# Optimization experiments

Hardware: AMD Instinct MI355X
Metric: run time of the kernel (lower is better)

## Reference

```python
import jax, jax.numpy as jnp
import numpy as np

K_NEIGHBORS = 32  # n_neighbors, eval mode -> displacement = 0


def setup_inputs() -> dict:
    key = jax.random.key(0)
    ks = jax.random.split(key, 9)
    B, N, F = 1024, 200000, 64
    C, H = 16, 128
    return {
        "x": jax.random.normal(ks[0], (B, F), jnp.float32),
        "X_data": jax.random.normal(ks[1], (N, F), jnp.float32),
        "y": jax.random.uniform(ks[2], (N,), jnp.float32),
        "W_gate": jax.random.normal(ks[3], (F + 1, C), jnp.float32) / np.sqrt(F + 1),
        "b_gate": jax.random.normal(ks[4], (C,), jnp.float32) * 0.01,
        "W1": jax.random.normal(ks[5], (C + F, H), jnp.float32) / np.sqrt(C + F),
        "b1": jax.random.normal(ks[6], (H,), jnp.float32) * 0.01,
        "W_last": jax.random.normal(ks[7], (H, 1), jnp.float32) / np.sqrt(H),
        "b_last": jax.random.normal(ks[8], (1,), jnp.float32) * 0.01,
    }


def reference(x, X_data, y, W_gate, b_gate, W1, b1, W_last, b_last):
    # Euclidean (p=2) cdist via the expanded form: ||a-b||^2 = ||a||^2 + ||b||^2 - 2 a.b
    d2 = (jnp.sum(x * x, axis=1, keepdims=True)
          + jnp.sum(X_data * X_data, axis=1)[None, :]
          - 2.0 * (x @ X_data.T))                      # [B, N]
    dist = jnp.sqrt(jnp.maximum(d2, 0.0))
    # torch.argsort(distances,1)[:, :k] == indices of k smallest distances
    _, idx = jax.lax.top_k(-dist, K_NEIGHBORS)          # [B, K]
    neighbors = X_data[idx]                             # [B, K, F] gather
    neighbors_y = y[idx][..., None]                     # [B, K, 1]
    nf = jnp.concatenate([neighbors, neighbors_y], axis=2)  # [B, K, F+1]
    gated = jnp.tanh(nf @ W_gate + b_gate)              # [B, K, C]
    agg = jnp.sum(gated, axis=1)                        # [B, C]
    o = jnp.concatenate([x, agg], axis=1)               # [B, F+C]
    o = jnp.tanh(o @ W1 + b1)                           # activation_function = tanh
    o = jax.nn.sigmoid(o @ W_last + b_last)             # [B, 1]
    return o
```

## Files before the change

### kernel.cpp

```cpp
#include <hip/hip_runtime.h>
#include <cstdint>

#define FDIM 64
#define KNN 32
#define NBUCKET 256
#define MAXCAP 2048
#define SEG 10
#define OCAP 512
#define BANDQ 96

typedef unsigned int u32;
typedef unsigned long long u64;
typedef __attribute__((ext_vector_type(8))) short bf16x8;
typedef __attribute__((ext_vector_type(4))) float f32x4;

__device__ __forceinline__ void gload_lds16(const void* g, void* l) {
    __builtin_amdgcn_global_load_lds(
        (const __attribute__((address_space(1))) unsigned int*)g,
        (__attribute__((address_space(3))) unsigned int*)l,
        16, 0, 0);
}

__device__ __forceinline__ float load_query(const float* __restrict__ x, int q, float4* xv) {
    const float4* xp = (const float4*)(x + (size_t)q * FDIM);
    float n0 = 0.f, n1 = 0.f, n2 = 0.f, n3 = 0.f;
#pragma unroll
    for (int k = 0; k < 16; ++k) {
        float4 v = xp[k];
        xv[k] = v;
        n0 = fmaf(v.x, v.x, n0); n1 = fmaf(v.y, v.y, n1);
        n2 = fmaf(v.z, v.z, n2); n3 = fmaf(v.w, v.w, n3);
    }
    return (n0 + n1) + (n2 + n3);
}

__device__ __forceinline__ float dot_row(const float4* __restrict__ xv, const float* __restrict__ row) {
    const float4* rv = (const float4*)row;
    float d0 = 0.f, d1 = 0.f, d2 = 0.f, d3 = 0.f;
#pragma unroll
    for (int k = 0; k < 16; ++k) {
        float4 r = rv[k];
        float4 a = xv[k];
        d0 = fmaf(a.x, r.x, d0); d1 = fmaf(a.y, r.y, d1);
        d2 = fmaf(a.z, r.z, d2); d3 = fmaf(a.w, r.w, d3);
    }
    return (d0 + d1) + (d2 + d3);
}

__global__ __launch_bounds__(256) void k_xnorm(const float* __restrict__ X, float* __restrict__ Xn, int N) {
    int i = blockIdx.x * 256 + threadIdx.x;
    if (i >= N) return;
    const float4* r = (const float4*)(X + (size_t)i * FDIM);
    float d0 = 0.f, d1 = 0.f, d2 = 0.f, d3 = 0.f;
#pragma unroll
    for (int k = 0; k < 16; ++k) {
        float4 v = r[k];
        d0 = fmaf(v.x, v.x, d0); d1 = fmaf(v.y, v.y, d1);
        d2 = fmaf(v.z, v.z, d2); d3 = fmaf(v.w, v.w, d3);
    }
    Xn[i] = (d0 + d1) + (d2 + d3);
}

__global__ __launch_bounds__(256) void k_cvtT(const float* __restrict__ src, uint4* __restrict__ dst, int n_u4) {
    int i = blockIdx.x * 256 + threadIdx.x;
    if (i >= n_u4) return;
    int lane = i & 63;
    int kk = (i >> 6) & 1;
    int g = i >> 7;
    int row = g * 16 + (lane & 15);
    int col = kk * 32 + (lane >> 4) * 8;
    const float4* s = (const float4*)(src + (size_t)row * FDIM + col);
    float4 a = s[0], b = s[1];
    ushort o[8];
    const float* f = &a.x;
#pragma unroll
    for (int k = 0; k < 4; ++k) {
        u32 u = __float_as_uint(f[k]);
        o[k] = (ushort)((u + 0x7fffu + ((u >> 16) & 1u)) >> 16);
    }
    const float* gg = &b.x;
#pragma unroll
    for (int k = 0; k < 4; ++k) {
        u32 u = __float_as_uint(gg[k]);
        o[4 + k] = (ushort)((u + 0x7fffu + ((u >> 16) & 1u)) >> 16);
    }
    dst[i] = *(uint4*)o;
}

__global__ __launch_bounds__(256) void k_hist(const float* __restrict__ x, const float* __restrict__ X,
                                              const float* __restrict__ Xn, u32* __restrict__ hist,
                                              int N, int nsamp, int sj) {
    __shared__ unsigned char h8[NBUCKET * 256];
    int t = threadIdx.x;
    u32* h32 = (u32*)h8;
#pragma unroll
    for (int k = 0; k < 64; ++k) h32[k * 256 + t] = 0;
    __syncthreads();
    int q = blockIdx.x * 256 + t;
    float4 xv[16];
    float xn = load_query(x, q, xv);
    for (int j = 0; j < sj; ++j) {
        int s = blockIdx.y * sj + j;
        int p = s * 16;
        if (s < nsamp && p < N) {
            float dp = dot_row(xv, X + (size_t)p * FDIM);
            float d2 = fmaxf(xn + Xn[p] - 2.f * dp, 0.f);
            int b = min(NBUCKET - 1, (int)d2);
            int idx = b * 256 + t;
            unsigned char v = h8[idx];
            h8[idx] = (v == 255u) ? v : (unsigned char)(v + 1);
        }
    }
    __syncthreads();
#pragma unroll
    for (int w = 0; w < 128; ++w) {
        u32 v0 = h8[(2 * w) * 256 + t];
        u32 v1 = h8[(2 * w + 1) * 256 + t];
        if (v0 | v1) atomicAdd(&hist[(size_t)q * 128 + w], v0 | (v1 << 16));
    }
}

__global__ __launch_bounds__(256) void k_thresh(const u32* __restrict__ hist, float* __restrict__ Tq, int B) {
    int q = blockIdx.x * 256 + threadIdx.x;
    if (q >= B) return;
    const u32* h = hist + (size_t)q * 128;
    int cum = 0;
    float T = (float)NBUCKET;
    for (int w = 0; w < 128; ++w) {
        u32 v = h[w];
        cum += (int)(v & 0xffffu);
        if (cum >= KNN) { T = (float)(2 * w + 1); break; }
        cum += (int)(v >> 16);
        if (cum >= KNN) { T = (float)(2 * w + 2); break; }
    }
    Tq[q] = T + 2.0f;
}

__global__ __launch_bounds__(256, 3) void k_sample_d2(
        const uint4* __restrict__ xT, const uint4* __restrict__ XT,
        const float* __restrict__ qn, const float* __restrict__ Xn,
        unsigned char* __restrict__ d2s, int S) {
    int t = threadIdx.x;
    int w = t >> 6, lane = t & 63;
    int G = lane >> 4, r = lane & 15;
    int qg = blockIdx.x;
    int wq = qg * 128 + w * 32;
    int pb = blockIdx.y * 128;

    bf16x8 afr[2][2];
#pragma unroll
    for (int kk = 0; kk < 2; ++kk)
#pragma unroll
        for (int mi = 0; mi < 2; ++mi) {
            uint4 v = xT[(size_t)(((wq >> 4) + mi) * 2 + kk) * 64 + lane];
            afr[kk][mi] = *(bf16x8*)&v;
        }
    float qr[8];
#pragma unroll
    for (int e = 0; e < 8; ++e)
        qr[e] = qn[wq + (e >> 2) * 16 + G * 4 + (e & 3)];

#pragma unroll
    for (int half = 0; half < 2; ++half) {
        int nb = half * 4;
        bf16x8 bfr[4][2];
#pragma unroll
        for (int j = 0; j < 4; ++j) {
            int gp = (pb >> 4) + nb + j;
#pragma unroll
            for (int kk = 0; kk < 2; ++kk) {
                uint4 v = XT[(size_t)(gp * 2 + kk) * 64 + lane];
                bfr[j][kk] = *(bf16x8*)&v;
            }
        }
        float xnv[4];
#pragma unroll
        for (int j = 0; j < 4; ++j) xnv[j] = Xn[pb + (nb + j) * 16 + r];

        f32x4 acc[2][4];
#pragma unroll
        for (int mi = 0; mi < 2; ++mi)
#pragma unroll
            for (int j = 0; j < 4; ++j) acc[mi][j] = (f32x4){0.f, 0.f, 0.f, 0.f};
#pragma unroll
        for (int kk = 0; kk < 2; ++kk)
#pragma unroll
            for (int j = 0; j < 4; ++j) {
                acc[0][j] = __builtin_amdgcn_mfma_f32_16x16x32_bf16(afr[kk][0], bfr[j][kk], acc[0][j], 0, 0, 0);
                acc[1][j] = __builtin_amdgcn_mfma_f32_16x16x32_bf16(afr[kk][1], bfr[j][kk], acc[1][j], 0, 0, 0);
            }
#pragma unroll
        for (int j = 0; j < 4; ++j) {
            int p = pb + (nb + j) * 16 + r;
            float xnp = xnv[j];
#pragma unroll
            for (int e = 0; e < 8; ++e) {
                float d2a = qr[e] + fmaf(-2.f, acc[e >> 2][j][e & 3], xnp);
                int b = (int)d2a;
                b = b < 0 ? 0 : (b > 255 ? 255 : b);
                int q = wq + (e >> 2) * 16 + G * 4 + (e & 3);
                d2s[(size_t)q * S + p] = (unsigned char)b;
            }
        }
    }
}

__global__ __launch_bounds__(256) void k_thresh2(const unsigned char* __restrict__ d2s,
                                                 float* __restrict__ Tq, int S) {
    __shared__ u32 h[NBUCKET];
    int t = threadIdx.x;
    int q = blockIdx.x;
    h[t] = 0;
    __syncthreads();
    const u32* row = (const u32*)(d2s + (size_t)q * S);
    int n4 = S >> 2;
    for (int i = t; i < n4; i += 256) {
        u32 v = row[i];
        atomicAdd(&h[v & 255u], 1u);
        atomicAdd(&h[(v >> 8) & 255u], 1u);
        atomicAdd(&h[(v >> 16) & 255u], 1u);
        atomicAdd(&h[v >> 24], 1u);
    }
    __syncthreads();
    if (t == 0) {
        int cum = 0;
        float T = 256.0f;
        for (int b = 0; b < NBUCKET; ++b) {
            cum += (int)h[b];
            if (cum >= KNN) { T = (float)(b + 1); break; }
        }
        Tq[q] = T + 2.0f;
    }
}

__global__ __launch_bounds__(256, 4) void k_mfma_filter(
        const uint4* __restrict__ xT, const uint4* __restrict__ XT,
        const float* __restrict__ qn, const float* __restrict__ Xn,
        const float* __restrict__ Tf,
        u32* __restrict__ cnt_seg, u32* __restrict__ list_seg,
        u32* __restrict__ ocnt, u32* __restrict__ olist,
        int N, int nStripsPad, int strip) {
    __shared__ uint4 sbuf[2][1024];
    __shared__ u32 ldsCnt[128];

    int t = threadIdx.x;
    int w = t >> 6, lane = t & 63;
    int G = lane >> 4, r = lane & 15;

    int bid = blockIdx.x;
    int qg = (bid >> 3) & 7;
    int sIdx = (bid & 7) | ((bid >> 6) << 3);
    int qbase = qg * 128;
    int wq = qbase + w * 32;

    if (t < 128) ldsCnt[t] = 0;
    __syncthreads();

    bf16x8 afr[2][2];
#pragma unroll
    for (int kk = 0; kk < 2; ++kk)
#pragma unroll
        for (int mi = 0; mi < 2; ++mi) {
            uint4 v = xT[(size_t)(((wq >> 4) + mi) * 2 + kk) * 64 + lane];
            afr[kk][mi] = *(bf16x8*)&v;
        }
    float nT[8], qnr[8];
#pragma unroll
    for (int e = 0; e < 8; ++e) {
        int rl = wq + (e >> 2) * 16 + G * 4 + (e & 3);
        float qv = qn[rl];
        qnr[e] = qv;
        nT[e] = -0.5f * (Tf[rl] - qv);
    }

    u32* segBase = list_seg + ((size_t)qbase * nStripsPad + (size_t)sIdx) * SEG;

    int pb0 = sIdx * strip * 128;
    int ntl = (pb0 < N) ? strip : 0;

    if (ntl > 0) {
        {
            const char* src = (const char*)XT + (size_t)(pb0 >> 4) * 2048 + w * 1024 + lane * 16;
            char* dst = (char*)&sbuf[0][0] + w * 1024;
            gload_lds16(src, dst);
            gload_lds16(src + 4096, dst + 4096);
            gload_lds16(src + 8192, dst + 8192);
            gload_lds16(src + 12288, dst + 12288);
        }
        __syncthreads();

        for (int s = 0; s < ntl; ++s) {
            int pb = pb0 + s * 128;
            if (s + 1 < ntl) {
                const char* src = (const char*)XT + (size_t)((pb + 128) >> 4) * 2048 + w * 1024 + lane * 16;
                char* dst = (char*)&sbuf[(s + 1) & 1][0] + w * 1024;
                gload_lds16(src, dst);
                gload_lds16(src + 4096, dst + 4096);
                gload_lds16(src + 8192, dst + 8192);
                gload_lds16(src + 12288, dst + 12288);
            }
            const uint4* cur = &sbuf[s & 1][0];

#pragma unroll
            for (int half = 0; half < 2; ++half) {
                int nb = half * 4;
                bf16x8 bfr[4][2];
#pragma unroll
                for (int j = 0; j < 4; ++j) {
#pragma unroll
                    for (int kk = 0; kk < 2; ++kk) {
                        uint4 v = cur[((nb + j) * 2 + kk) * 64 + lane];
                        bfr[j][kk] = *(bf16x8*)&v;
                    }
                }
                float xnv[4], ai[4];
#pragma unroll
                for (int j = 0; j < 4; ++j) {
                    xnv[j] = Xn[pb + (nb + j) * 16 + r];
                    ai[j] = -0.5f * xnv[j];
                }

                f32x4 acc[2][4];
#pragma unroll
                for (int mi = 0; mi < 2; ++mi)
#pragma unroll
                    for (int j = 0; j < 4; ++j) acc[mi][j] = (f32x4){ai[j], ai[j], ai[j], ai[j]};
#pragma unroll
                for (int kk = 0; kk < 2; ++kk)
#pragma unroll
                    for (int j = 0; j < 4; ++j) {
                        acc[0][j] = __builtin_amdgcn_mfma_f32_16x16x32_bf16(afr[kk][0], bfr[j][kk], acc[0][j], 0, 0, 0);
                        acc[1][j] = __builtin_amdgcn_mfma_f32_16x16x32_bf16(afr[kk][1], bfr[j][kk], acc[1][j], 0, 0, 0);
                    }
#pragma unroll
                for (int j = 0; j < 4; ++j) {
                    int p = pb + (nb + j) * 16 + r;
                    bool ce[8];
#pragma unroll
                    for (int e = 0; e < 8; ++e)
                        ce[e] = acc[e >> 2][j][e & 3] > nT[e];
                    if ((ce[0] | ce[1] | ce[2] | ce[3] | ce[4] | ce[5] | ce[6] | ce[7]) && p < N) {
#pragma unroll
                        for (int e = 0; e < 8; ++e) {
                            if (ce[e]) {
                                float d2a = fmaf(-2.f, acc[e >> 2][j][e & 3], qnr[e]);
                                d2a = d2a < 0.f ? 0.f : d2a;
                                u32 dq = (u32)(d2a * 32.f);
                                if (dq > 16383u) dq = 16383u;
                                u32 key = (dq << 18) | (u32)p;
                                int ql = w * 32 + (e >> 2) * 16 + G * 4 + (e & 3);
                                u32 slot = atomicAdd(&ldsCnt[ql], 1u);
                                if (slot < SEG) {
                                    segBase[(size_t)ql * nStripsPad * SEG + slot] = key;
                                } else {
                                    u32 gs = atomicAdd(&ocnt[qbase + ql], 1u);
                                    if (gs < OCAP) olist[(size_t)(qbase + ql) * OCAP + gs] = key;
                                }
                            }
                        }
                    }
                }
            }
            __syncthreads();
        }
    }

    __syncthreads();
    if (t < 128) cnt_seg[(size_t)(qbase + t) * nStripsPad + sIdx] = min(ldsCnt[t], (u32)SEG);
}

__global__ __launch_bounds__(256) void k_filter_scalar(const float* __restrict__ x, const float* __restrict__ X,
                                                       const float* __restrict__ Xn, const float* __restrict__ Tq,
                                                       u32* __restrict__ cnt, u32* __restrict__ list,
                                                       int N, int cap) {
    int t = threadIdx.x;
    int q = blockIdx.x * 256 + t;
    float4 xv[16];
    float xn = load_query(x, q, xv);
    float T = Tq[q];
    int base = blockIdx.y * 1024;
    int lim = min(1024, N - base);
    for (int j = 0; j < lim; ++j) {
        int p = base + j;
        float dp = dot_row(xv, X + (size_t)p * FDIM);
        float d2 = fmaxf(xn + Xn[p] - 2.f * dp, 0.f);
        if (d2 < T) {
            u32 slot = atomicAdd(&cnt[q], 1u);
            if (slot < (u32)cap) list[(size_t)q * cap + slot] = (u32)p;
        }
    }
}

__global__ __launch_bounds__(256) void k_final(const float* __restrict__ x, const float* __restrict__ X,
                                               const float* __restrict__ y, const float* __restrict__ Xn,
                                               const float* __restrict__ Wg, const float* __restrict__ bg,
                                               const float* __restrict__ W1, const float* __restrict__ b1,
                                               const float* __restrict__ Wl, const float* __restrict__ bl,
                                               const u32* __restrict__ cnt_seg, const u32* __restrict__ list_seg,
                                               const u32* __restrict__ ocnt, const u32* __restrict__ olist,
                                               const u32* __restrict__ cnt_flat, const u32* __restrict__ list_flat,
                                               float* __restrict__ out, int nStripsPad, int cap_flat, int flat,
                                               int N) {
    __shared__ u64 keys[MAXCAP];
    __shared__ u32 nsh;
    __shared__ u64 wk[4];
    __shared__ int wp[4];
    __shared__ u32 sel[KNN];
    __shared__ float gkc[KNN * 16];
    __shared__ float aggc[16];
    __shared__ float red[128];
    __shared__ u32 hist[2048];
    __shared__ u32 wtot[4];
    __shared__ u32 cutq_sh;
    __shared__ u32 nrs;

    int t = threadIdx.x;
    int w = t >> 6, lane = t & 63;
    int q = blockIdx.x;
    int m;

    if (flat) {
        m = (int)min(cnt_flat[q], (u32)cap_flat);
        const u32* lq = list_flat + (size_t)q * cap_flat;
        for (int i = t; i < m; i += 256) keys[i] = lq[i];
    } else {
        if (t == 0) nsh = 0;
        __syncthreads();
        for (int seg = t; seg < nStripsPad; seg += 256) {
            u32 c = cnt_seg[(size_t)q * nStripsPad + seg];
            if (c) {
                u32 base = atomicAdd(&nsh, c);
                const u32* sp = list_seg + ((size_t)q * nStripsPad + seg) * SEG;
                for (u32 j = 0; j < c; ++j) {
                    u32 idx = base + j;
                    if (idx < MAXCAP) keys[idx] = sp[j];
                }
            }
        }
        __syncthreads();
        int m0 = (int)min(nsh, (u32)MAXCAP);
        int oc = (int)min(ocnt[q], (u32)OCAP);
        for (int i = t; i < oc; i += 256)
            if (m0 + i < MAXCAP) keys[m0 + i] = olist[(size_t)q * OCAP + i];
        m = min(m0 + oc, MAXCAP);
    }
    __syncthreads();

    if (!flat) {
        for (int i = t; i < 2048; i += 256) hist[i] = 0;
        if (t == 0) cutq_sh = 0xFFFFFFFFu;
        __syncthreads();
        for (int i = t; i < m; i += 256) atomicAdd(&hist[((u32)keys[i]) >> 21], 1u);
        __syncthreads();
        u32 s = 0;
#pragma unroll
        for (int j = 0; j < 8; ++j) s += hist[t * 8 + j];
        u32 run = s;
#pragma unroll
        for (int off = 1; off < 64; off <<= 1) {
            u32 v = __shfl_up(run, off);
            if (lane >= off) run += v;
        }
        if (lane == 63) wtot[w] = run;
        __syncthreads();
        u32 wo = 0;
#pragma unroll
        for (int v = 0; v < 4; ++v) wo += (v < w) ? wtot[v] : 0u;
        u32 inc = wo + run;
        u32 exc = inc - s;
        if (exc < (u32)KNN && inc >= (u32)KNN) {
            u32 cum = exc;
#pragma unroll
            for (int j = 0; j < 8; ++j) {
                cum += hist[t * 8 + j];
                if (cum >= (u32)KNN) { cutq_sh = (u32)(((t * 8 + j + 1) << 3) + BANDQ); break; }
            }
        }
    }
    if (t == 0) nrs = 0;
    __syncthreads();
    u32 cutq = flat ? 0xFFFFFFFFu : cutq_sh;

    u32* cand = hist;
    for (int i = t; i < m; i += 256) {
        u32 k = (u32)keys[i];
        if ((k >> 18) <= cutq) cand[atomicAdd(&nrs, 1u)] = k & 0x3FFFFu;
    }
    __syncthreads();
    int mr = (int)min(nrs, (u32)MAXCAP);

    {
        int ch = lane & 15;
        int rsub = lane >> 4;
        float4 xq4 = ((const float4*)(x + (size_t)q * FDIM))[ch];
        float xs = fmaf(xq4.x, xq4.x, fmaf(xq4.y, xq4.y, fmaf(xq4.z, xq4.z, xq4.w * xq4.w)));
        xs += __shfl_xor(xs, 1);
        xs += __shfl_xor(xs, 2);
        xs += __shfl_xor(xs, 4);
        xs += __shfl_xor(xs, 8);
        float xn = xs;
        for (int base = w * 32; base < mr; base += 128) {
            int ri[8]; u32 pp[8]; bool val[8]; float4 vv[8];
#pragma unroll
            for (int u = 0; u < 8; ++u) {
                ri[u] = base + u * 4 + rsub;
                val[u] = ri[u] < mr;
                pp[u] = val[u] ? cand[ri[u]] : 0u;
            }
#pragma unroll
            for (int u = 0; u < 8; ++u)
                vv[u] = ((const float4*)(X + (size_t)pp[u] * FDIM))[ch];
#pragma unroll
            for (int u = 0; u < 8; ++u) {
                float part = fmaf(xq4.x, vv[u].x, fmaf(xq4.y, vv[u].y, fmaf(xq4.z, vv[u].z, xq4.w * vv[u].w)));
                part += __shfl_xor(part, 1);
                part += __shfl_xor(part, 2);
                part += __shfl_xor(part, 4);
                part += __shfl_xor(part, 8);
                if (val[u] && ch == 0) {
                    float d2 = fmaxf(xn + Xn[pp[u]] - 2.f * part, 0.f);
                    keys[ri[u]] = ((u64)__float_as_uint(d2) << 32) | pp[u];
                }
            }
        }
    }
    __syncthreads();

    if (mr <= 512) {
        if (w == 0) {
            u64 rk[8];
#pragma unroll
            for (int i = 0; i < 8; ++i) {
                int idx = lane + (i << 6);
                rk[i] = (idx < mr) ? keys[idx] : ~0ull;
            }
            for (int r = 0; r < KNN; ++r) {
                u64 bk = ~0ull;
                int bs = 0;
#pragma unroll
                for (int i = 0; i < 8; ++i)
                    if (rk[i] < bk) { bk = rk[i]; bs = i; }
                int bo = lane;
#pragma unroll
                for (int off = 1; off < 64; off <<= 1) {
                    u64 ok = __shfl_xor(bk, off);
                    int oo = __shfl_xor(bo, off);
                    if (ok < bk) { bk = ok; bo = oo; }
                }
                if (lane == bo) rk[bs] = ~0ull;
                if (lane == 0) sel[r] = (u32)bk;
            }
        }
        __syncthreads();
    } else {
        for (int r = 0; r < KNN; ++r) {
            u64 bk = ~0ull;
            int bp = -1;
            for (int i = t; i < mr; i += 256) {
                u64 k = keys[i];
                if (k < bk) { bk = k; bp = i; }
            }
#pragma unroll
            for (int off = 32; off > 0; off >>= 1) {
                u64 ok = __shfl_down(bk, off);
                int op = __shfl_down(bp, off);
                if (ok < bk) { bk = ok; bp = op; }
            }
            if (lane == 0) { wk[w] = bk; wp[w] = bp; }
            __syncthreads();
            if (t == 0) {
                u64 fb = wk[0];
                int fp = wp[0];
                for (int v = 1; v < 4; ++v)
                    if (wk[v] < fb) { fb = wk[v]; fp = wp[v]; }
                sel[r] = (u32)(fb & 0xffffffffu);
                if (fp >= 0) keys[fp] = ~0ull;
            }
            __syncthreads();
        }
    }

    int c = t & 15, kk = t >> 4;
#pragma unroll
    for (int rep = 0; rep < 2; ++rep) {
        int k = kk + 16 * rep;
        int nb = min((int)sel[k], N - 1);
        const float* Xr = X + (size_t)nb * FDIM;
        float acc = bg[c];
#pragma unroll
        for (int f = 0; f < FDIM; ++f) acc = fmaf(Xr[f], Wg[f * 16 + c], acc);
        acc = fmaf(y[nb], Wg[FDIM * 16 + c], acc);
        gkc[k * 16 + c] = tanhf(acc);
    }
    __syncthreads();
    if (t < 16) {
        float s = 0.f;
#pragma unroll
        for (int k = 0; k < KNN; ++k) s += gkc[k * 16 + t];
        aggc[t] = s;
    }
    __syncthreads();
    if (t < 128) {
        const float* xq = x + (size_t)q * FDIM;
        float acc = b1[t];
#pragma unroll
        for (int f = 0; f < FDIM; ++f) acc = fmaf(xq[f], W1[f * 128 + t], acc);
#pragma unroll
        for (int cc2 = 0; cc2 < 16; ++cc2) acc = fmaf(aggc[cc2], W1[(FDIM + cc2) * 128 + t], acc);
        red[t] = tanhf(acc) * Wl[t];
    }
    __syncthreads();
    for (int off = 64; off > 0; off >>= 1) {
        if (t < off) red[t] += red[t + off];
        __syncthreads();
    }
    if (t == 0) out[q] = 1.f / (1.f + expf(-(red[0] + bl[0])));
}

extern "C" void kernel_launch(void* const* d_in, const int* in_sizes, int n_in,
                              void* d_out, int out_size, void* d_ws, size_t ws_size,
                              hipStream_t stream) {
    const float* x  = (const float*)d_in[0];
    const float* X  = (const float*)d_in[1];
    const float* y  = (const float*)d_in[2];
    const float* Wg = (const float*)d_in[3];
    const float* bg = (const float*)d_in[4];
    const float* W1 = (const float*)d_in[5];
    const float* b1 = (const float*)d_in[6];
    const float* Wl = (const float*)d_in[7];
    const float* bl = (const float*)d_in[8];
    float* out = (float*)d_out;

    int B = in_sizes[0] / FDIM;
    int N = in_sizes[1] / FDIM;

    const int strip = 8;
    int nTiles = (N + 127) / 128;
    int nStrips = (nTiles + strip - 1) / strip;
    nStrips = (nStrips + 7) & ~7;
    int nStripsPad = nStrips;
    int Npad = nStrips * strip * 128;

    char* w = (char*)d_ws;
    size_t off = 0;
    auto alloc = [&](size_t bytes) { void* p = w + off; off += (bytes + 255) & ~(size_t)255; return p; };
    float* Xn  = (float*)alloc((size_t)Npad * 4);
    float* qn  = (float*)alloc((size_t)B * 4);
    u32* hist  = (u32*)alloc((size_t)B * 512);
    float* Tq  = (float*)alloc((size_t)B * 4);
    u32* cnt   = (u32*)alloc((size_t)B * 4);

    size_t xTB = (size_t)B * 128;
    size_t XTB = (size_t)(Npad / 16) * 2048;
    size_t segCntB = (size_t)B * nStripsPad * 4;
    size_t segListB = (size_t)B * nStripsPad * SEG * 4;
    size_t ocntB = (size_t)B * 4;
    size_t olistB = (size_t)B * OCAP * 4;
    size_t rem = (ws_size > off) ? ws_size - off : 0;
    bool mfma_path = rem >= xTB + XTB + segCntB + segListB + ocntB + olistB + 4096;

    uint4* xT = nullptr; uint4* XT = nullptr;
    u32 *cnt_seg = nullptr, *list_seg = nullptr, *ocnt = nullptr, *olist = nullptr;
    u32* list_flat = nullptr; unsigned char* d2s = nullptr;
    int cap_flat = 64, Stiles = 0;
    if (mfma_path) {
        xT = (uint4*)alloc(xTB);
        XT = (uint4*)alloc(XTB);
        cnt_seg  = (u32*)alloc(segCntB);
        list_seg = (u32*)alloc(segListB);
        ocnt     = (u32*)alloc(ocntB);
        olist    = (u32*)alloc(olistB);
        rem = (ws_size > off) ? ws_size - off : 0;
        size_t st = rem / ((size_t)B * 128);
        Stiles = st > 198 ? 198 : (int)st;
        int maxFull = N / 128;
        if (Stiles > maxFull) Stiles = maxFull;
        if (Stiles >= 96) d2s = (unsigned char*)alloc((size_t)Stiles * 128 * B);
        else Stiles = 0;
    } else {
        size_t c = rem / ((size_t)B * 4);
        cap_flat = c > MAXCAP ? MAXCAP : (int)c;
        if (cap_flat < 64) cap_flat = 64;
        list_flat = (u32*)alloc((size_t)B * cap_flat * 4);
    }

    k_xnorm<<<dim3((N + 255) / 256), 256, 0, stream>>>(X, Xn, N);
    k_xnorm<<<dim3((B + 255) / 256), 256, 0, stream>>>(x, qn, B);

    if (mfma_path) {
        hipMemsetAsync(ocnt, 0, ocntB, stream);
        hipMemsetAsync(Xn + N, 0, (size_t)(Npad - N) * 4, stream);
        size_t realXT = (size_t)(N / 16) * 2048;
        hipMemsetAsync((char*)XT + realXT, 0, XTB - realXT, stream);

        int nxu4 = B * 8, nXu4 = N * 8;
        k_cvtT<<<dim3((nxu4 + 255) / 256), 256, 0, stream>>>(x, xT, nxu4);
        k_cvtT<<<dim3((nXu4 + 255) / 256), 256, 0, stream>>>(X, XT, nXu4);

        if (Stiles > 0) {
            int S = Stiles * 128;
            k_sample_d2<<<dim3(8, Stiles), 256, 0, stream>>>(xT, XT, qn, Xn, d2s, S);
            k_thresh2<<<dim3(B), 256, 0, stream>>>(d2s, Tq, S);
        } else {
            hipMemsetAsync(hist, 0, (size_t)B * 512, stream);
            int nsamp = (N + 15) / 16;
            int chunks = 128;
            int sj = (nsamp + chunks - 1) / chunks;
            k_hist<<<dim3(B / 256, chunks), 256, 0, stream>>>(x, X, Xn, hist, N, nsamp, sj);
            k_thresh<<<dim3((B + 255) / 256), 256, 0, stream>>>(hist, Tq, B);
        }

        k_mfma_filter<<<dim3(8 * nStrips), 256, 0, stream>>>(
            xT, XT, qn, Xn, Tq, cnt_seg, list_seg, ocnt, olist, N, nStripsPad, strip);

        k_final<<<dim3(B), 256, 0, stream>>>(x, X, y, Xn, Wg, bg, W1, b1, Wl, bl,
                                             cnt_seg, list_seg, ocnt, olist,
                                             nullptr, nullptr, out, nStripsPad, 0, 0, N);
    } else {
        hipMemsetAsync(cnt, 0, (size_t)B * 4, stream);
        hipMemsetAsync(hist, 0, (size_t)B * 512, stream);
        int nsamp = (N + 15) / 16;
        int chunks = 128;
        int sj = (nsamp + chunks - 1) / chunks;
        k_hist<<<dim3(B / 256, chunks), 256, 0, stream>>>(x, X, Xn, hist, N, nsamp, sj);
        k_thresh<<<dim3((B + 255) / 256), 256, 0, stream>>>(hist, Tq, B);
        k_filter_scalar<<<dim3(B / 256, (N + 1023) / 1024), 256, 0, stream>>>(
            x, X, Xn, Tq, cnt, list_flat, N, cap_flat);
        k_final<<<dim3(B), 256, 0, stream>>>(x, X, y, Xn, Wg, bg, W1, b1, Wl, bl,
                                             nullptr, nullptr, nullptr, nullptr,
                                             cnt, list_flat, out, nStripsPad, cap_flat, 1, N);
    }
}
```

Baseline: 261.8 us.

## Fuse norm computation into bf16 transpose conversion and retune strip/sample sizes

Adds a k_cvtT_norm kernel that computes per-row squared norms while converting rows to the bf16 tiled layout. This removes the separate k_xnorm passes over X and x on the MFMA path, so the 51MB data matrix is read once instead of twice. It also halves the strip width, lowers SEG from 10 to 8, and caps the threshold-sampling tiles at 100 instead of 198. The smaller sample set may give looser per-query thresholds and more surviving candidates, and the narrower strips double the per-strip segment bookkeeping.

Result: faster. 245.4 us (-6.3%).

```diff
diff --git a/kernel.cpp b/kernel.cpp
--- a/kernel.cpp
+++ b/kernel.cpp
@@ -5,7 +5,7 @@
 #define KNN 32
 #define NBUCKET 256
 #define MAXCAP 2048
-#define SEG 10
+#define SEG 8
 #define OCAP 512
 #define BANDQ 96
 
@@ -85,6 +85,49 @@
         o[4 + k] = (ushort)((u + 0x7fffu + ((u >> 16) & 1u)) >> 16);
     }
     dst[i] = *(uint4*)o;
+}
+
+__global__ __launch_bounds__(256) void k_cvtT_norm(const float* __restrict__ src, uint4* __restrict__ dst,
+                                                   float* __restrict__ norms, int n_u4) {
+    __shared__ float pn[4][16];
+    int t = threadIdx.x;
+    int i = blockIdx.x * 256 + t;
+    int lane = t & 63;
+    int w = t >> 6;
+    int kk = (i >> 6) & 1;
+    int g = i >> 7;
+    int r = lane & 15;
+    int row = g * 16 + r;
+    int col = kk * 32 + (lane >> 4) * 8;
+    const float4* s = (const float4*)(src + (size_t)row * FDIM + col);
+    float4 a = s[0], b = s[1];
+    float n0 = fmaf(a.x, a.x, a.y * a.y);
+    float n1 = fmaf(a.z, a.z, a.w * a.w);
+    float n2 = fmaf(b.x, b.x, b.y * b.y);
+    float n3 = fmaf(b.z, b.z, b.w * b.w);
+    float ss = (n0 + n1) + (n2 + n3);
+    ushort o[8];
+    const float* f = &a.x;
+#pragma unroll
+    for (int k = 0; k < 4; ++k) {
+        u32 u = __float_as_uint(f[k]);
+        o[k] = (ushort)((u + 0x7fffu + ((u >> 16) & 1u)) >> 16);
+    }
+    const float* gg = &b.x;
+#pragma unroll
+    for (int k = 0; k < 4; ++k) {
+        u32 u = __float_as_uint(gg[k]);
+        o[4 + k] = (ushort)((u + 0x7fffu + ((u >> 16) & 1u)) >> 16);
+    }
+    dst[i] = *(uint4*)o;
+    ss += __shfl_xor(ss, 16);
+    ss += __shfl_xor(ss, 32);
+    if (lane < 16) pn[w][r] = ss;
+    __syncthreads();
+    if (t < 32) {
+        float v = (t < 16) ? (pn[0][t] + pn[1][t]) : (pn[2][t - 16] + pn[3][t - 16]);
+        norms[blockIdx.x * 32 + t] = v;
+    }
 }
 
 __global__ __launch_bounds__(256) void k_hist(const float* __restrict__ x, const float* __restrict__ X,
@@ -634,7 +677,7 @@
     int B = in_sizes[0] / FDIM;
     int N = in_sizes[1] / FDIM;
 
-    const int strip = 8;
+    const int strip = 4;
     int nTiles = (N + 127) / 128;
     int nStrips = (nTiles + strip - 1) / strip;
     nStrips = (nStrips + 7) & ~7;
@@ -672,7 +715,7 @@
         olist    = (u32*)alloc(olistB);
         rem = (ws_size > off) ? ws_size - off : 0;
         size_t st = rem / ((size_t)B * 128);
-        Stiles = st > 198 ? 198 : (int)st;
+        Stiles = st > 100 ? 100 : (int)st;
         int maxFull = N / 128;
         if (Stiles > maxFull) Stiles = maxFull;
         if (Stiles >= 96) d2s = (unsigned char*)alloc((size_t)Stiles * 128 * B);
@@ -684,9 +727,6 @@
         list_flat = (u32*)alloc((size_t)B * cap_flat * 4);
     }
 
-    k_xnorm<<<dim3((N + 255) / 256), 256, 0, stream>>>(X, Xn, N);
-    k_xnorm<<<dim3((B + 255) / 256), 256, 0, stream>>>(x, qn, B);
-
     if (mfma_path) {
         hipMemsetAsync(ocnt, 0, ocntB, stream);
         hipMemsetAsync(Xn + N, 0, (size_t)(Npad - N) * 4, stream);
@@ -694,8 +734,18 @@
         hipMemsetAsync((char*)XT + realXT, 0, XTB - realXT, stream);
 
         int nxu4 = B * 8, nXu4 = N * 8;
-        k_cvtT<<<dim3((nxu4 + 255) / 256), 256, 0, stream>>>(x, xT, nxu4);
-        k_cvtT<<<dim3((nXu4 + 255) / 256), 256, 0, stream>>>(X, XT, nXu4);
+        if ((nxu4 & 255) == 0) {
+            k_cvtT_norm<<<dim3(nxu4 / 256), 256, 0, stream>>>(x, xT, qn, nxu4);
+        } else {
+            k_xnorm<<<dim3((B + 255) / 256), 256, 0, stream>>>(x, qn, B);
+            k_cvtT<<<dim3((nxu4 + 255) / 256), 256, 0, stream>>>(x, xT, nxu4);
+        }
+        if ((nXu4 & 255) == 0) {
+            k_cvtT_norm<<<dim3(nXu4 / 256), 256, 0, stream>>>(X, XT, Xn, nXu4);
+        } else {
+            k_xnorm<<<dim3((N + 255) / 256), 256, 0, stream>>>(X, Xn, N);
+            k_cvtT<<<dim3((nXu4 + 255) / 256), 256, 0, stream>>>(X, XT, nXu4);
+        }
 
         if (Stiles > 0) {
             int S = Stiles * 128;
@@ -717,6 +767,8 @@
                                              cnt_seg, list_seg, ocnt, olist,
                                              nullptr, nullptr, out, nStripsPad, 0, 0, N);
     } else {
+        k_xnorm<<<dim3((N + 255) / 256), 256, 0, stream>>>(X, Xn, N);
+        k_xnorm<<<dim3((B + 255) / 256), 256, 0, stream>>>(x, qn, B);
         hipMemsetAsync(cnt, 0, (size_t)B * 4, stream);
         hipMemsetAsync(hist, 0, (size_t)B * 512, stream);
         int nsamp = (N + 15) / 16;
```
